# Kernel tuning notes

Measured on AMD Instinct MI355X. Metric: run time of the kernel, lower is better.

Reference implementation:

```python
import jax, jax.numpy as jnp
import numpy as np

M = 4                 # margin order (init kwarg m=4)
LAMB = 1000.0         # it=0: max(lambda_min, lambda_max/(1+gamma*0)**power) = 1000
B, D, C = 512, 256, 100000


def setup_inputs() -> dict:
    key = jax.random.key(0)
    k1, k2, k3 = jax.random.split(key, 3)
    x = jax.random.normal(k1, (B, D), dtype=jnp.float32)
    # kaiming_uniform_(weight, a=1.0): bound = sqrt(6/((1+a^2)*fan_in)) = sqrt(3/D)
    bound = float(np.sqrt(3.0 / D))
    weight = jax.random.uniform(k2, (C, D), dtype=jnp.float32, minval=-bound, maxval=bound)
    y = jax.random.randint(k3, (B,), 0, C)
    return {"x": x, "weight": weight, "y": y}


def reference(x, weight, y):
    # weight row-normalization (normalize=True path, done in-place in torch)
    wl = jnp.sqrt(jnp.sum(weight * weight, axis=1, keepdims=True))
    w = weight / wl                                  # (C, D), unit rows -> wlen == 1
    xlen = jnp.sqrt(jnp.sum(x * x, axis=1, keepdims=True))   # (B, 1)
    cos = jnp.clip((x @ w.T) / xlen, -1.0, 1.0)      # (B, C) cos_theta
    # m=4 Chebyshev: cos(4t) = 8c^4 - 8c^2 + 1
    c2 = cos * cos
    cos_m = 8.0 * c2 * c2 - 8.0 * c2 + 1.0
    k = jnp.floor(M * jnp.arccos(cos) / jnp.pi)      # (B, C)
    sign = 1.0 - 2.0 * (k % 2.0)                     # (-1)**k
    phi = sign * cos_m - 2.0 * k
    feat = cos * xlen
    onehot = jax.nn.one_hot(y, w.shape[0], dtype=feat.dtype)  # (B, C)
    # at label positions: feat <- (lamb*feat + phi*xlen) / (1+lamb)
    feat = feat + onehot * ((phi * xlen - feat) / (1.0 + LAMB))
    return feat
```

## Files before the change

kernel.cpp:

```cpp
#include <hip/hip_runtime.h>
#include <hip/hip_bf16.h>

#define B_DIM 512
#define D_DIM 256
#define C_DIM 100000
#define LAMB 1000.0f

using bf16x8 = __attribute__((ext_vector_type(8))) short;
using f32x4  = __attribute__((ext_vector_type(4))) float;

__device__ __forceinline__ short f2bf(float f) {
  unsigned u = __builtin_bit_cast(unsigned, f);
  u += 0x7FFFu + ((u >> 16) & 1u);
  return (short)(u >> 16);
}

__global__ __launch_bounds__(256) void prep_x(const float* __restrict__ x,
                                              unsigned short* __restrict__ x_swz,
                                              float* __restrict__ xlen) {
  int wv = threadIdx.x >> 6, lane = threadIdx.x & 63;
  int row = blockIdx.x * 4 + wv;
  float4 v = *(const float4*)(x + row * D_DIM + lane * 4);
  float ss = v.x * v.x + v.y * v.y + v.z * v.z + v.w * v.w;
#pragma unroll
  for (int m = 1; m < 64; m <<= 1) ss += __shfl_xor(ss, m);
  if (lane == 0) xlen[row] = sqrtf(ss);
  ushort4 u;
  u.x = (unsigned short)f2bf(v.x);
  u.y = (unsigned short)f2bf(v.y);
  u.z = (unsigned short)f2bf(v.z);
  u.w = (unsigned short)f2bf(v.w);
  int byteoff = row * 512 + ((lane * 8) ^ ((row & 7) << 4));
  *(ushort4*)((char*)x_swz + byteoff) = u;
}

__global__ __launch_bounds__(256) void gemm_bf16(
    const float* __restrict__ W, const unsigned short* __restrict__ x_swz,
    const float* __restrict__ xlen, float* __restrict__ out) {
  __shared__ unsigned short xs[64 * 256];
  __shared__ float xlen_s[B_DIM];

  const int tid = threadIdx.x;
  const int lane = tid & 63, wv = tid >> 6;
  const int l15 = lane & 15, g = lane >> 4;
  const int bn0 = blockIdx.x * 128 + wv * 32;

  for (int i = tid; i < B_DIM; i += 256) xlen_s[i] = xlen[i];

  bf16x8 fb[2][8];
  float invwl[2];
#pragma unroll
  for (int ns = 0; ns < 2; ++ns) {
    int col = bn0 + ns * 16 + l15;
    if (col >= C_DIM) col = C_DIM - 1;
    const float* wr = W + (size_t)col * D_DIM + g * 8;
    float ss = 0.f;
#pragma unroll
    for (int kg = 0; kg < 8; ++kg) {
      float4 a = *(const float4*)(wr + kg * 32);
      float4 b = *(const float4*)(wr + kg * 32 + 4);
      ss += a.x * a.x + a.y * a.y + a.z * a.z + a.w * a.w
          + b.x * b.x + b.y * b.y + b.z * b.z + b.w * b.w;
      bf16x8 f;
      f[0] = f2bf(a.x); f[1] = f2bf(a.y); f[2] = f2bf(a.z); f[3] = f2bf(a.w);
      f[4] = f2bf(b.x); f[5] = f2bf(b.y); f[6] = f2bf(b.z); f[7] = f2bf(b.w);
      fb[ns][kg] = f;
    }
    ss += __shfl_xor(ss, 16);
    ss += __shfl_xor(ss, 32);
    invwl[ns] = 1.0f / sqrtf(ss);
  }

  for (int chunk = 0; chunk < 8; ++chunk) {
    __syncthreads();
    {
      const int4* src = (const int4*)x_swz + chunk * 2048;
      int4* dst = (int4*)xs;
#pragma unroll
      for (int i = 0; i < 8; ++i) dst[i * 256 + tid] = src[i * 256 + tid];
    }
    __syncthreads();

    f32x4 acc[4][2] = {};
#pragma unroll
    for (int kg = 0; kg < 8; ++kg) {
      bf16x8 fa[4];
#pragma unroll
      for (int m = 0; m < 4; ++m) {
        int row = m * 16 + l15;
        int off = row * 512 + ((kg * 64 + g * 16) ^ ((row & 7) << 4));
        fa[m] = *(const bf16x8*)((const char*)xs + off);
      }
#pragma unroll
      for (int m = 0; m < 4; ++m)
#pragma unroll
        for (int ns = 0; ns < 2; ++ns)
          acc[m][ns] = __builtin_amdgcn_mfma_f32_16x16x32_bf16(
              fa[m], fb[ns][kg], acc[m][ns], 0, 0, 0);
    }

#pragma unroll
    for (int m = 0; m < 4; ++m) {
#pragma unroll
      for (int ns = 0; ns < 2; ++ns) {
        int col = bn0 + ns * 16 + l15;
        if (col < C_DIM) {
#pragma unroll
          for (int r = 0; r < 4; ++r) {
            int row = chunk * 64 + m * 16 + g * 4 + r;
            float xl = xlen_s[row];
            float v = acc[m][ns][r] * invwl[ns];
            v = fminf(fmaxf(v, -xl), xl);
            out[(size_t)row * C_DIM + col] = v;
          }
        }
      }
    }
  }
}

__global__ __launch_bounds__(256) void fix_labels(const float* __restrict__ x,
                                                  const float* __restrict__ W,
                                                  const int* __restrict__ y,
                                                  float* __restrict__ out) {
  int wv = threadIdx.x >> 6, lane = threadIdx.x & 63;
  int b = blockIdx.x * 4 + wv;
  int c = y[b];
  float4 wvv = *(const float4*)(W + (size_t)c * D_DIM + lane * 4);
  float4 xv  = *(const float4*)(x + b * D_DIM + lane * 4);
  float dt = wvv.x * xv.x + wvv.y * xv.y + wvv.z * xv.z + wvv.w * xv.w;
  float sw = wvv.x * wvv.x + wvv.y * wvv.y + wvv.z * wvv.z + wvv.w * wvv.w;
  float sx = xv.x * xv.x + xv.y * xv.y + xv.z * xv.z + xv.w * xv.w;
#pragma unroll
  for (int m = 1; m < 64; m <<= 1) {
    dt += __shfl_xor(dt, m);
    sw += __shfl_xor(sw, m);
    sx += __shfl_xor(sx, m);
  }
  if (lane == 0) {
    float xl = sqrtf(sx), wl = sqrtf(sw);
    float cth = dt / (xl * wl);
    cth = fminf(fmaxf(cth, -1.f), 1.f);
    float c2 = cth * cth;
    float cm = 8.f * c2 * c2 - 8.f * c2 + 1.f;
    float k = floorf(4.0f * acosf(cth) / 3.14159265358979323846f);
    float sgn = (((int)k) & 1) ? -1.f : 1.f;
    float phi = sgn * cm - 2.f * k;
    float feat = cth * xl;
    out[(size_t)b * C_DIM + c] = feat + (phi * xl - feat) / (1.f + LAMB);
  }
}

extern "C" void kernel_launch(void* const* d_in, const int* in_sizes, int n_in,
                              void* d_out, int out_size, void* d_ws, size_t ws_size,
                              hipStream_t stream) {
  const float* x = (const float*)d_in[0];
  const float* W = (const float*)d_in[1];
  const int*   y = (const int*)d_in[2];
  float* out = (float*)d_out;

  unsigned short* x_swz = (unsigned short*)d_ws;
  float* xlen = (float*)((char*)d_ws + B_DIM * D_DIM * 2);

  prep_x<<<B_DIM / 4, 256, 0, stream>>>(x, x_swz, xlen);
  gemm_bf16<<<(C_DIM + 127) / 128, 256, 0, stream>>>(W, x_swz, xlen, out);
  fix_labels<<<B_DIM / 4, 256, 0, stream>>>(x, W, y, out);
}
```

Baseline: 94.24 us.

## Swap MFMA operands to emit float4 stores and read x directly from global

Swaps the MFMA operand roles so W rows map to the output rows of each 16x16 tile. Each lane then holds four consecutive output columns and can write them with one float4 store instead of scalar stores. The shared-memory staging of x, its swizzle and the block barriers are dropped; each wave instead loads 16 bf16 x rows straight from global memory, where they should stay cached in L2, across 32 iterations. This trades LDS reuse for more global/L2 reads of x, with fewer MFMAs per x load.

After: 180.3 us. 1.91x slower.

```diff
diff --git a/kernel.cpp b/kernel.cpp
--- a/kernel.cpp
+++ b/kernel.cpp
@@ -16,7 +16,7 @@
 }
 
 __global__ __launch_bounds__(256) void prep_x(const float* __restrict__ x,
-                                              unsigned short* __restrict__ x_swz,
+                                              unsigned short* __restrict__ xb,
                                               float* __restrict__ xlen) {
   int wv = threadIdx.x >> 6, lane = threadIdx.x & 63;
   int row = blockIdx.x * 4 + wv;
@@ -30,28 +30,22 @@
   u.y = (unsigned short)f2bf(v.y);
   u.z = (unsigned short)f2bf(v.z);
   u.w = (unsigned short)f2bf(v.w);
-  int byteoff = row * 512 + ((lane * 8) ^ ((row & 7) << 4));
-  *(ushort4*)((char*)x_swz + byteoff) = u;
+  *(ushort4*)(xb + row * D_DIM + lane * 4) = u;
 }
 
 __global__ __launch_bounds__(256) void gemm_bf16(
-    const float* __restrict__ W, const unsigned short* __restrict__ x_swz,
+    const float* __restrict__ W, const unsigned short* __restrict__ xb,
     const float* __restrict__ xlen, float* __restrict__ out) {
-  __shared__ unsigned short xs[64 * 256];
-  __shared__ float xlen_s[B_DIM];
-
   const int tid = threadIdx.x;
   const int lane = tid & 63, wv = tid >> 6;
   const int l15 = lane & 15, g = lane >> 4;
   const int bn0 = blockIdx.x * 128 + wv * 32;
 
-  for (int i = tid; i < B_DIM; i += 256) xlen_s[i] = xlen[i];
-
-  bf16x8 fb[2][8];
-  float invwl[2];
+  bf16x8 fw[2][8];
+  float invw4[2][4];
 #pragma unroll
-  for (int ns = 0; ns < 2; ++ns) {
-    int col = bn0 + ns * 16 + l15;
+  for (int it = 0; it < 2; ++it) {
+    int col = bn0 + it * 16 + l15;
     if (col >= C_DIM) col = C_DIM - 1;
     const float* wr = W + (size_t)col * D_DIM + g * 8;
     float ss = 0.f;
@@ -64,56 +58,42 @@
       bf16x8 f;
       f[0] = f2bf(a.x); f[1] = f2bf(a.y); f[2] = f2bf(a.z); f[3] = f2bf(a.w);
       f[4] = f2bf(b.x); f[5] = f2bf(b.y); f[6] = f2bf(b.z); f[7] = f2bf(b.w);
-      fb[ns][kg] = f;
+      fw[it][kg] = f;
     }
     ss += __shfl_xor(ss, 16);
     ss += __shfl_xor(ss, 32);
-    invwl[ns] = 1.0f / sqrtf(ss);
+    float iw = 1.0f / sqrtf(ss);
+#pragma unroll
+    for (int r = 0; r < 4; ++r) invw4[it][r] = __shfl(iw, g * 4 + r);
   }
 
-  for (int chunk = 0; chunk < 8; ++chunk) {
-    __syncthreads();
-    {
-      const int4* src = (const int4*)x_swz + chunk * 2048;
-      int4* dst = (int4*)xs;
+  for (int jt = 0; jt < 32; ++jt) {
+    const int xrow = jt * 16 + l15;
+    float xl = xlen[xrow];
+    const unsigned short* xp = xb + xrow * D_DIM + g * 8;
+    bf16x8 fx[8];
 #pragma unroll
-      for (int i = 0; i < 8; ++i) dst[i * 256 + tid] = src[i * 256 + tid];
-    }
-    __syncthreads();
+    for (int kg = 0; kg < 8; ++kg)
+      fx[kg] = *(const bf16x8*)(xp + kg * 32);
 
-    f32x4 acc[4][2] = {};
+    f32x4 acc0 = {}, acc1 = {};
 #pragma unroll
     for (int kg = 0; kg < 8; ++kg) {
-      bf16x8 fa[4];
-#pragma unroll
-      for (int m = 0; m < 4; ++m) {
-        int row = m * 16 + l15;
-        int off = row * 512 + ((kg * 64 + g * 16) ^ ((row & 7) << 4));
-        fa[m] = *(const bf16x8*)((const char*)xs + off);
-      }
-#pragma unroll
-      for (int m = 0; m < 4; ++m)
-#pragma unroll
-        for (int ns = 0; ns < 2; ++ns)
-          acc[m][ns] = __builtin_amdgcn_mfma_f32_16x16x32_bf16(
-              fa[m], fb[ns][kg], acc[m][ns], 0, 0, 0);
+      acc0 = __builtin_amdgcn_mfma_f32_16x16x32_bf16(fw[0][kg], fx[kg], acc0, 0, 0, 0);
+      acc1 = __builtin_amdgcn_mfma_f32_16x16x32_bf16(fw[1][kg], fx[kg], acc1, 0, 0, 0);
     }
 
 #pragma unroll
-    for (int m = 0; m < 4; ++m) {
-#pragma unroll
-      for (int ns = 0; ns < 2; ++ns) {
-        int col = bn0 + ns * 16 + l15;
-        if (col < C_DIM) {
-#pragma unroll
-          for (int r = 0; r < 4; ++r) {
-            int row = chunk * 64 + m * 16 + g * 4 + r;
-            float xl = xlen_s[row];
-            float v = acc[m][ns][r] * invwl[ns];
-            v = fminf(fmaxf(v, -xl), xl);
-            out[(size_t)row * C_DIM + col] = v;
-          }
-        }
+    for (int it = 0; it < 2; ++it) {
+      const f32x4& a = it ? acc1 : acc0;
+      int wc = bn0 + it * 16 + g * 4;
+      if (wc < C_DIM) {
+        float4 v;
+        v.x = fminf(fmaxf(a[0] * invw4[it][0], -xl), xl);
+        v.y = fminf(fmaxf(a[1] * invw4[it][1], -xl), xl);
+        v.z = fminf(fmaxf(a[2] * invw4[it][2], -xl), xl);
+        v.w = fminf(fmaxf(a[3] * invw4[it][3], -xl), xl);
+        *(float4*)(out + (size_t)xrow * C_DIM + wc) = v;
       }
     }
   }
@@ -159,10 +139,10 @@
   const int*   y = (const int*)d_in[2];
   float* out = (float*)d_out;
 
-  unsigned short* x_swz = (unsigned short*)d_ws;
+  unsigned short* xb = (unsigned short*)d_ws;
   float* xlen = (float*)((char*)d_ws + B_DIM * D_DIM * 2);
 
-  prep_x<<<B_DIM / 4, 256, 0, stream>>>(x, x_swz, xlen);
-  gemm_bf16<<<(C_DIM + 127) / 128, 256, 0, stream>>>(W, x_swz, xlen, out);
+  prep_x<<<B_DIM / 4, 256, 0, stream>>>(x, xb, xlen);
+  gemm_bf16<<<(C_DIM + 127) / 128, 256, 0, stream>>>(W, xb, xlen, out);
   fix_labels<<<B_DIM / 4, 256, 0, stream>>>(x, W, y, out);
 }
```
